# Optimization experiments

Hardware: AMD Instinct MI355X
Metric: run time of the kernel (lower is better)

Reference implementation:

```python
import jax, jax.numpy as jnp
import numpy as np
import math

D_MODEL = 512
N_HEADS = 8
D_FF = 2048
EPS = 1e-5

def _layernorm(x, g, b):
    m = jnp.mean(x, axis=-1, keepdims=True)
    v = jnp.var(x, axis=-1, keepdims=True)
    return (x - m) * jax.lax.rsqrt(v + EPS) * g + b

def setup_inputs() -> dict:
    key = jax.random.key(0)
    ks = jax.random.split(key, 8)
    d, dff = D_MODEL, D_FF
    s = lambda fan: 1.0 / math.sqrt(fan)
    return {
        "x": jax.random.normal(ks[0], (4, 2048, d), dtype=jnp.float32),
        "w_qkv": jax.random.normal(ks[1], (d, 3 * d), dtype=jnp.float32) * s(d),
        "b_qkv": jnp.zeros((3 * d,), dtype=jnp.float32),
        "w1": jax.random.normal(ks[2], (d, dff), dtype=jnp.float32) * s(d),
        "b1": jnp.zeros((dff,), dtype=jnp.float32),
        "w2": jax.random.normal(ks[3], (dff, d), dtype=jnp.float32) * s(dff),
        "b2": jnp.zeros((d,), dtype=jnp.float32),
        "g1": jnp.ones((d,), dtype=jnp.float32),
        "be1": jnp.zeros((d,), dtype=jnp.float32),
        "g2": jnp.ones((d,), dtype=jnp.float32),
        "be2": jnp.zeros((d,), dtype=jnp.float32),
    }

def reference(x, w_qkv, b_qkv, w1, b1, w2, b2, g1, be1, g2, be2):
    B, L, d = x.shape
    H = N_HEADS
    hd = d // H
    # Faithful to original: scale = 1/sqrt(hd), scores = qk / scale = qk * sqrt(hd)
    inv_scale = math.sqrt(hd)
    qkv = x @ w_qkv + b_qkv            # [B, L, 3d]
    q, k, v = jnp.split(qkv, 3, axis=-1)
    split_heads = lambda t: t.reshape(B, L, H, hd).transpose(0, 2, 1, 3)  # [B,H,L,hd]
    q, k, v = map(split_heads, (q, k, v))
    scores = jnp.einsum('bhqd,bhkd->bhqk', q, k) * inv_scale
    attn = jax.nn.softmax(scores, axis=-1)
    out = jnp.einsum('bhqk,bhkd->bhqd', attn, v)
    out = out.transpose(0, 2, 1, 3).reshape(B, L, d)
    x = _layernorm(x + out, g1, be1)
    ff = jax.nn.relu(x @ w1 + b1) @ w2 + b2
    return _layernorm(x + ff, g2, be2)
```

## Files before the change

kernel.cpp:

```cpp
#include <hip/hip_runtime.h>

typedef _Float16 f16;
typedef _Float16 f16x4 __attribute__((ext_vector_type(4)));
typedef _Float16 f16x8 __attribute__((ext_vector_type(8)));
typedef float    f32x4 __attribute__((ext_vector_type(4)));
typedef float    f32x16 __attribute__((ext_vector_type(16)));
typedef unsigned int u32x4 __attribute__((ext_vector_type(4)));

#define QK_SCALE 11.5416528f

__device__ __forceinline__ void g2l16(const void* g, void* l) {
  __builtin_amdgcn_global_load_lds(
      (__attribute__((address_space(1))) const unsigned int*)g,
      (__attribute__((address_space(3))) unsigned int*)l, 16, 0, 0);
}

__device__ __forceinline__ f32x4 mfma16(f16x8 a, f16x8 b, f32x4 c) {
  return __builtin_amdgcn_mfma_f32_16x16x32_f16(a, b, c, 0, 0, 0);
}
__device__ __forceinline__ f32x16 mfma32(f16x8 a, f16x8 b, f32x16 c) {
  return __builtin_amdgcn_mfma_f32_32x32x16_f16(a, b, c, 0, 0, 0);
}
__device__ __forceinline__ unsigned pkrtz(float a, float b) {
  auto t = __builtin_amdgcn_cvt_pkrtz(a, b);
  return *(unsigned*)&t;
}
__device__ __forceinline__ void swap32(unsigned& a, unsigned& b) {
  asm volatile("v_permlane32_swap_b32 %0, %1" : "+v"(a), "+v"(b));
}

__device__ __forceinline__ int swz64(int row, int c) { return row * 64 + ((c ^ (row & 7)) << 3); }
__device__ __forceinline__ int swz32(int row, int c) { return row * 32 + ((c ^ ((row >> 1) & 3)) << 3); }

__global__ __launch_bounds__(256) void k_split(const float* __restrict__ in,
                                               f16* __restrict__ hi, f16* __restrict__ lo, int n4) {
  int i = blockIdx.x * 256 + threadIdx.x;
  if (i >= n4) return;
  f32x4 v = ((const f32x4*)in)[i];
  f16x4 h, l;
#pragma unroll
  for (int j = 0; j < 4; ++j) {
    f16 hv = (f16)v[j];
    h[j] = hv;
    l[j] = (f16)(v[j] - (float)hv);
  }
  ((f16x4*)hi)[i] = h;
  ((f16x4*)lo)[i] = l;
}

template <bool WLO>
__global__ __launch_bounds__(256) void k_transpose_split(const float* __restrict__ in, int K, int N,
                                                         f16* __restrict__ oh, f16* __restrict__ ol) {
  __shared__ float t[32][33];
  const int tx = threadIdx.x, ty = threadIdx.y;
  const int n0 = blockIdx.x * 32, k0 = blockIdx.y * 32;
#pragma unroll
  for (int j = 0; j < 4; ++j)
    t[ty + j * 8][tx] = in[(size_t)(k0 + ty + j * 8) * N + n0 + tx];
  __syncthreads();
#pragma unroll
  for (int j = 0; j < 4; ++j) {
    float v = t[tx][ty + j * 8];
    f16 hv = (f16)v;
    size_t o = (size_t)(n0 + ty + j * 8) * K + k0 + tx;
    oh[o] = hv;
    if (WLO) ol[o] = (f16)(v - (float)hv);
  }
}

template <int EPI, bool SPLIT>
__global__ __launch_bounds__(256, SPLIT ? 2 : 3) void k_gemm(
    const f16* __restrict__ Ah, const f16* __restrict__ Al,
    const f16* __restrict__ Bh, const f16* __restrict__ Bl,
    const float* __restrict__ bias,
    float* __restrict__ outF, f16* __restrict__ outH,
    f16* __restrict__ oqh, f16* __restrict__ oql,
    f16* __restrict__ okh, f16* __restrict__ ovT,
    int M, int N, int K) {
  constexpr int NB = SPLIT ? 2 : 1;
  __shared__ f16 As[NB][128 * 32];
  __shared__ f16 Bs[NB][128 * 32];

  const int tid = threadIdx.x;
  const int bm = blockIdx.x, bn = blockIdx.y;
  const int w = tid >> 6, lane = tid & 63;
  const int wr = w >> 1, wc = w & 1;
  const int lrow = lane & 15, lgrp = lane >> 4;

  const bool useLo = SPLIT && !(EPI == 0 && bn >= 8);

  f32x4 acc[4][4] = {};

  const int nkt = K >> 5;
  for (int kt = 0; kt < nkt; ++kt) {
    __syncthreads();
    const int kk = kt << 5;
#pragma unroll
    for (int c = 0; c < 2; ++c) {
      const int i = tid + (c << 8);
      const int row = i >> 2;
      const int gch = ((i & 3) ^ ((i >> 3) & 3)) << 3;
      const size_t aoff = (size_t)(bm * 128 + row) * K + kk + gch;
      const size_t boff = (size_t)(bn * 128 + row) * K + kk + gch;
      g2l16(Ah + aoff, &As[0][i * 8]);
      g2l16(Bh + boff, &Bs[0][i * 8]);
      if (SPLIT)
        if (useLo) {
          g2l16(Al + aoff, &As[1][i * 8]);
          g2l16(Bl + boff, &Bs[1][i * 8]);
        }
    }
    __syncthreads();

    f16x8 a0[4], a1[4], b0[4], b1[4];
#pragma unroll
    for (int mf = 0; mf < 4; ++mf) {
      const int off = swz32(wr * 64 + mf * 16 + lrow, lgrp);
      a0[mf] = *(const f16x8*)&As[0][off];
      if (SPLIT)
        if (useLo) a1[mf] = *(const f16x8*)&As[SPLIT ? 1 : 0][off];
    }
#pragma unroll
    for (int nf = 0; nf < 4; ++nf) {
      const int off = swz32(wc * 64 + nf * 16 + lrow, lgrp);
      b0[nf] = *(const f16x8*)&Bs[0][off];
      if (SPLIT)
        if (useLo) b1[nf] = *(const f16x8*)&Bs[SPLIT ? 1 : 0][off];
    }
#pragma unroll
    for (int mf = 0; mf < 4; ++mf)
#pragma unroll
      for (int nf = 0; nf < 4; ++nf) {
        acc[mf][nf] = mfma16(a0[mf], b0[nf], acc[mf][nf]);
        if (SPLIT)
          if (useLo) {
            acc[mf][nf] = mfma16(a0[mf], b1[nf], acc[mf][nf]);
            acc[mf][nf] = mfma16(a1[mf], b0[nf], acc[mf][nf]);
          }
      }
  }

  const int rowbase = bm * 128 + wr * 64 + lgrp * 4;
  const int colbase = bn * 128 + wc * 64 + lrow;
#pragma unroll
  for (int mf = 0; mf < 4; ++mf) {
#pragma unroll
    for (int nf = 0; nf < 4; ++nf) {
      const int gc = colbase + nf * 16;
      const float bv = bias[gc];
#pragma unroll
      for (int r = 0; r < 4; ++r) {
        const int gr = rowbase + mf * 16 + r;
        const float val = acc[mf][nf][r] + bv;
        if (EPI == 0) {
          const int bb = gr >> 11, tok = gr & 2047;
          const int kind = gc >> 9, hh = (gc >> 6) & 7, dd = gc & 63;
          const size_t bhp = (size_t)((bb << 3) + hh);
          const size_t qidx = (bhp * 2048 + tok) * 64 + dd;
          if (kind == 0) {
            const float sv = val * QK_SCALE;
            const f16 hv = (f16)sv;
            oqh[qidx] = hv; oql[qidx] = (f16)(sv - (float)hv);
          } else if (kind == 1) {
            okh[qidx] = (f16)val;
          } else {
            ovT[(bhp * 64 + dd) * 2048 + tok] = (f16)val;
          }
        } else if (EPI == 1) {
          outH[(size_t)gr * N + gc] = (f16)fmaxf(val, 0.f);
        } else {
          outF[(size_t)gr * N + gc] = val;
        }
      }
    }
  }
}

__global__ __launch_bounds__(256, 2) void k_attn(
    const f16* __restrict__ Qh, const f16* __restrict__ Ql,
    const f16* __restrict__ Kh, const f16* __restrict__ Vt,
    float* __restrict__ out) {
  __shared__ f16 sK[3][64 * 64], sV[3][64 * 64];

  const int tid = threadIdx.x;
  const int wg = (blockIdx.x & 7) * 64 + (blockIdx.x >> 3);
  const int bh = wg >> 4, qt = wg & 15;
  const int w = tid >> 6, lane = tid & 63;
  const int lh = lane & 31, hh = lane >> 5;

  auto stage = [&](int b, int kt) {
    const size_t koff = ((size_t)bh * 2048 + (size_t)kt * 64) * 64;
    const size_t voff = (size_t)bh * 64 * 2048 + (size_t)kt * 64;
#pragma unroll
    for (int c = 0; c < 2; ++c) {
      const int i = tid + (c << 8);
      const int row = i >> 3;
      const int gch = ((i & 7) ^ (row & 7)) << 3;
      g2l16(Kh + koff + (size_t)row * 64 + gch, &sK[b][i * 8]);
      g2l16(Vt + voff + (size_t)row * 2048 + gch, &sV[b][i * 8]);
    }
  };

  stage(0, 0);
  stage(1, 1);

  const int qrow = qt * 128 + w * 32 + lh;
  const size_t qoff = ((size_t)bh * 2048 + qrow) * 64;
  f16x8 qh8[4], ql8[4];
#pragma unroll
  for (int d = 0; d < 4; ++d) {
    const size_t o = qoff + d * 16 + hh * 8;
    qh8[d] = *(const f16x8*)(Qh + o);
    ql8[d] = *(const f16x8*)(Ql + o);
  }

  float m_run = -3e38f;
  float l_run = 0.f;
  f32x16 oacc[2] = {};

  asm volatile("s_waitcnt vmcnt(4)" ::: "memory");
  __builtin_amdgcn_sched_barrier(0);
  __builtin_amdgcn_s_barrier();

  for (int kt = 0; kt < 32; ++kt) {
    const int cur = kt - (kt / 3) * 3;
    if (kt < 30) {
      const int nxt = (kt + 2) - ((kt + 2) / 3) * 3;
      stage(nxt, kt + 2);
    }

    f32x16 s[2] = {};
    __builtin_amdgcn_s_setprio(1);
#pragma unroll
    for (int d = 0; d < 4; ++d) {
      const f16x8 k0 = *(const f16x8*)&sK[cur][swz64(lh, d * 2 + hh)];
      const f16x8 k1 = *(const f16x8*)&sK[cur][swz64(32 + lh, d * 2 + hh)];
      s[0] = mfma32(k0, qh8[d], s[0]);
      s[0] = mfma32(k0, ql8[d], s[0]);
      s[1] = mfma32(k1, qh8[d], s[1]);
      s[1] = mfma32(k1, ql8[d], s[1]);
    }
    __builtin_amdgcn_s_setprio(0);

    float mt = s[0][0];
#pragma unroll
    for (int r = 0; r < 16; ++r) { mt = fmaxf(mt, s[0][r]); mt = fmaxf(mt, s[1][r]); }
    mt = fmaxf(mt, __shfl_xor(mt, 32, 64));
    float mcur = m_run;
    if (!__all(mt <= mcur + 8.0f)) {
      const float mnew = fmaxf(mcur, mt);
      const float corr = __builtin_amdgcn_exp2f(mcur - mnew);
      m_run = mnew;
      l_run *= corr;
      oacc[0] = oacc[0] * corr;
      oacc[1] = oacc[1] * corr;
      mcur = mnew;
    }
    float ps = 0.f;
    unsigned pk0[8], pk1[8];
#pragma unroll
    for (int i = 0; i < 8; ++i) {
      const float a0 = __builtin_amdgcn_exp2f(s[0][2 * i] - mcur);
      const float a1 = __builtin_amdgcn_exp2f(s[0][2 * i + 1] - mcur);
      const float b0 = __builtin_amdgcn_exp2f(s[1][2 * i] - mcur);
      const float b1 = __builtin_amdgcn_exp2f(s[1][2 * i + 1] - mcur);
      ps += (a0 + a1) + (b0 + b1);
      pk0[i] = pkrtz(a0, a1);
      pk1[i] = pkrtz(b0, b1);
    }
    ps += __shfl_xor(ps, 32, 64);
    l_run += ps;

    swap32(pk0[0], pk0[2]); swap32(pk0[1], pk0[3]);
    swap32(pk0[4], pk0[6]); swap32(pk0[5], pk0[7]);
    swap32(pk1[0], pk1[2]); swap32(pk1[1], pk1[3]);
    swap32(pk1[4], pk1[6]); swap32(pk1[5], pk1[7]);

    u32x4 pbu[4];
    pbu[0] = (u32x4){pk0[0], pk0[1], pk0[2], pk0[3]};
    pbu[1] = (u32x4){pk0[4], pk0[5], pk0[6], pk0[7]};
    pbu[2] = (u32x4){pk1[0], pk1[1], pk1[2], pk1[3]};
    pbu[3] = (u32x4){pk1[4], pk1[5], pk1[6], pk1[7]};

    __builtin_amdgcn_s_setprio(1);
#pragma unroll
    for (int s2 = 0; s2 < 4; ++s2) {
      const f16x8 pb = *(const f16x8*)&pbu[s2];
#pragma unroll
      for (int db = 0; db < 2; ++db) {
        const f16x8 v = *(const f16x8*)&sV[cur][swz64(db * 32 + lh, s2 * 2 + hh)];
        oacc[db] = mfma32(v, pb, oacc[db]);
      }
    }
    __builtin_amdgcn_s_setprio(0);

    if (kt < 30) {
      asm volatile("s_waitcnt vmcnt(4)" ::: "memory");
    } else {
      asm volatile("s_waitcnt vmcnt(0)" ::: "memory");
    }
    __builtin_amdgcn_sched_barrier(0);
    __builtin_amdgcn_s_barrier();
  }

  const int b = bh >> 3, hd = bh & 7;
  const float inv = 1.0f / l_run;
  const int trow = b * 2048 + qt * 128 + w * 32 + lh;
  float* po = out + (size_t)trow * 512 + hd * 64;
#pragma unroll
  for (int db = 0; db < 2; ++db)
#pragma unroll
    for (int rq = 0; rq < 4; ++rq) {
      f32x4 o;
#pragma unroll
      for (int j = 0; j < 4; ++j) o[j] = oacc[db][rq * 4 + j] * inv;
      *(f32x4*)(po + db * 32 + rq * 8 + hh * 4) = o;
    }
}

__global__ __launch_bounds__(64) void k_ln(const float* __restrict__ X, const float* __restrict__ R,
                                           const float* __restrict__ g, const float* __restrict__ be,
                                           float* __restrict__ outF, f16* __restrict__ outH) {
  const int row = blockIdx.x, t = threadIdx.x;
  const size_t base = (size_t)row * 512 + t * 8;
  f32x4 x0 = *(const f32x4*)(X + base);
  f32x4 x1 = *(const f32x4*)(X + base + 4);
  f32x4 r0 = *(const f32x4*)(R + base);
  f32x4 r1 = *(const f32x4*)(R + base + 4);
  x0 = x0 + r0;
  x1 = x1 + r1;
  float s = 0.f, ss = 0.f;
#pragma unroll
  for (int j = 0; j < 4; ++j) { s += x0[j] + x1[j]; ss += x0[j] * x0[j] + x1[j] * x1[j]; }
#pragma unroll
  for (int o = 32; o; o >>= 1) {
    s += __shfl_xor(s, o, 64);
    ss += __shfl_xor(ss, o, 64);
  }
  const float mean = s * (1.f / 512.f);
  const float var = ss * (1.f / 512.f) - mean * mean;
  const float rs = rsqrtf(var + 1e-5f);
  f32x4 g0 = *(const f32x4*)(g + t * 8);
  f32x4 g1v = *(const f32x4*)(g + t * 8 + 4);
  f32x4 b0 = *(const f32x4*)(be + t * 8);
  f32x4 b1 = *(const f32x4*)(be + t * 8 + 4);
  f32x4 y0 = (x0 - mean) * rs * g0 + b0;
  f32x4 y1 = (x1 - mean) * rs * g1v + b1;
  *(f32x4*)(outF + base) = y0;
  *(f32x4*)(outF + base + 4) = y1;
  if (outH != nullptr) {
    f16x8 hx;
#pragma unroll
    for (int j = 0; j < 4; ++j) { hx[j] = (f16)y0[j]; hx[j + 4] = (f16)y1[j]; }
    *(f16x8*)(outH + base) = hx;
  }
}

extern "C" void kernel_launch(void* const* d_in, const int* in_sizes, int n_in,
                              void* d_out, int out_size, void* d_ws, size_t ws_size,
                              hipStream_t stream) {
  (void)in_sizes; (void)n_in; (void)out_size;
  const float* x = (const float*)d_in[0];
  const float* w_qkv = (const float*)d_in[1];
  const float* b_qkv = (const float*)d_in[2];
  const float* w1 = (const float*)d_in[3];
  const float* b1 = (const float*)d_in[4];
  const float* w2 = (const float*)d_in[5];
  const float* b2 = (const float*)d_in[6];
  const float* g1 = (const float*)d_in[7];
  const float* be1 = (const float*)d_in[8];
  const float* g2 = (const float*)d_in[9];
  const float* be2 = (const float*)d_in[10];
  float* out = (float*)d_out;

  char* p = (char*)d_ws;
  auto take = [&](size_t bytes) {
    char* r = p;
    p += (bytes + 255) & ~(size_t)255;
    return r;
  };
  f16* xh = (f16*)take(8192ull * 512 * 2);
  f16* xl = (f16*)take(8192ull * 512 * 2);
  f16* wqkvTh = (f16*)take(1536ull * 512 * 2);
  f16* wqkvTl = (f16*)take(1536ull * 512 * 2);
  f16* w1T = (f16*)take(2048ull * 512 * 2);
  f16* w2T = (f16*)take(512ull * 2048 * 2);
  f16* qh = (f16*)take(32ull * 2048 * 64 * 2);
  f16* ql = (f16*)take(32ull * 2048 * 64 * 2);
  f16* kh = (f16*)take(32ull * 2048 * 64 * 2);
  f16* vT = (f16*)take(32ull * 64 * 2048 * 2);
  float* attn = (float*)take(8192ull * 512 * 4);
  float* x1f = (float*)take(8192ull * 512 * 4);
  f16* x1h = (f16*)take(8192ull * 512 * 2);
  f16* hbuf = qh;
  float* ffb = attn;

  if ((size_t)(p - (char*)d_ws) > ws_size) return;

  dim3 tb(32, 8);
  k_split<<<4096, 256, 0, stream>>>(x, xh, xl, 8192 * 512 / 4);
  k_transpose_split<true><<<dim3(1536 / 32, 512 / 32), tb, 0, stream>>>(w_qkv, 512, 1536, wqkvTh, wqkvTl);
  k_transpose_split<false><<<dim3(2048 / 32, 512 / 32), tb, 0, stream>>>(w1, 512, 2048, w1T, nullptr);
  k_transpose_split<false><<<dim3(512 / 32, 2048 / 32), tb, 0, stream>>>(w2, 2048, 512, w2T, nullptr);

  k_gemm<0, true><<<dim3(64, 12), 256, 0, stream>>>(xh, xl, wqkvTh, wqkvTl, b_qkv,
                                                    nullptr, nullptr, qh, ql, kh, vT,
                                                    8192, 1536, 512);
  k_attn<<<512, 256, 0, stream>>>(qh, ql, kh, vT, attn);
  k_ln<<<8192, 64, 0, stream>>>(x, attn, g1, be1, x1f, x1h);
  k_gemm<1, false><<<dim3(64, 16), 256, 0, stream>>>(x1h, nullptr, w1T, nullptr, b1,
                                                     nullptr, hbuf, nullptr, nullptr, nullptr, nullptr,
                                                     8192, 2048, 512);
  k_gemm<2, false><<<dim3(64, 4), 256, 0, stream>>>(hbuf, nullptr, w2T, nullptr, b2,
                                                    ffb, nullptr, nullptr, nullptr, nullptr, nullptr,
                                                    8192, 512, 2048);
  k_ln<<<8192, 64, 0, stream>>>(x1f, ffb, g2, be2, out, nullptr);
}
```

Before: 201.9 us.

## Software-pipeline QK^T ahead of softmax/PV with 4-deep K/V staging in attention

The attention loop is restructured so the QK^T MFMAs for the next key tile are issued before the softmax and PV of the current tile. This uses two score accumulators and a 4-buffer LDS ring prefetching three tiles ahead, and the Q register loads are moved ahead of the initial staging. The aim is to overlap matrix-core work with the exp/max VALU work and hide more global-load latency. In exchange it costs more LDS and registers, which may lower occupancy. Separately, the QKV GEMM now skips the low-part split for output columns from bn>=4 instead of bn>=8, which drops some correction MFMAs but may reduce precision for those columns.

Measured after the change: 194.1 us. -3.9%, faster.

```diff
diff --git a/kernel.cpp b/kernel.cpp
--- a/kernel.cpp
+++ b/kernel.cpp
@@ -87,7 +87,7 @@
   const int wr = w >> 1, wc = w & 1;
   const int lrow = lane & 15, lgrp = lane >> 4;
 
-  const bool useLo = SPLIT && !(EPI == 0 && bn >= 8);
+  const bool useLo = SPLIT && !(EPI == 0 && bn >= 4);
 
   f32x4 acc[4][4] = {};
 
@@ -180,13 +180,23 @@
     const f16* __restrict__ Qh, const f16* __restrict__ Ql,
     const f16* __restrict__ Kh, const f16* __restrict__ Vt,
     float* __restrict__ out) {
-  __shared__ f16 sK[3][64 * 64], sV[3][64 * 64];
+  __shared__ f16 sK[4][64 * 64], sV[4][64 * 64];
 
   const int tid = threadIdx.x;
   const int wg = (blockIdx.x & 7) * 64 + (blockIdx.x >> 3);
   const int bh = wg >> 4, qt = wg & 15;
   const int w = tid >> 6, lane = tid & 63;
   const int lh = lane & 31, hh = lane >> 5;
+
+  const int qrow = qt * 128 + w * 32 + lh;
+  const size_t qoff = ((size_t)bh * 2048 + qrow) * 64;
+  f16x8 qh8[4], ql8[4];
+#pragma unroll
+  for (int d = 0; d < 4; ++d) {
+    const size_t o = qoff + d * 16 + hh * 8;
+    qh8[d] = *(const f16x8*)(Qh + o);
+    ql8[d] = *(const f16x8*)(Ql + o);
+  }
 
   auto stage = [&](int b, int kt) {
     const size_t koff = ((size_t)bh * 2048 + (size_t)kt * 64) * 64;
@@ -203,45 +213,28 @@
 
   stage(0, 0);
   stage(1, 1);
-
-  const int qrow = qt * 128 + w * 32 + lh;
-  const size_t qoff = ((size_t)bh * 2048 + qrow) * 64;
-  f16x8 qh8[4], ql8[4];
-#pragma unroll
-  for (int d = 0; d < 4; ++d) {
-    const size_t o = qoff + d * 16 + hh * 8;
-    qh8[d] = *(const f16x8*)(Qh + o);
-    ql8[d] = *(const f16x8*)(Ql + o);
-  }
+  stage(2, 2);
 
   float m_run = -3e38f;
   float l_run = 0.f;
   f32x16 oacc[2] = {};
-
-  asm volatile("s_waitcnt vmcnt(4)" ::: "memory");
-  __builtin_amdgcn_sched_barrier(0);
-  __builtin_amdgcn_s_barrier();
-
-  for (int kt = 0; kt < 32; ++kt) {
-    const int cur = kt - (kt / 3) * 3;
-    if (kt < 30) {
-      const int nxt = (kt + 2) - ((kt + 2) / 3) * 3;
-      stage(nxt, kt + 2);
-    }
-
-    f32x16 s[2] = {};
+  f32x16 sA[2] = {}, sB[2] = {};
+
+  auto qk = [&](f32x16 (&s)[2], int bi) {
     __builtin_amdgcn_s_setprio(1);
 #pragma unroll
     for (int d = 0; d < 4; ++d) {
-      const f16x8 k0 = *(const f16x8*)&sK[cur][swz64(lh, d * 2 + hh)];
-      const f16x8 k1 = *(const f16x8*)&sK[cur][swz64(32 + lh, d * 2 + hh)];
+      const f16x8 k0 = *(const f16x8*)&sK[bi][swz64(lh, d * 2 + hh)];
+      const f16x8 k1 = *(const f16x8*)&sK[bi][swz64(32 + lh, d * 2 + hh)];
       s[0] = mfma32(k0, qh8[d], s[0]);
       s[0] = mfma32(k0, ql8[d], s[0]);
       s[1] = mfma32(k1, qh8[d], s[1]);
       s[1] = mfma32(k1, ql8[d], s[1]);
     }
     __builtin_amdgcn_s_setprio(0);
-
+  };
+
+  auto sm_pv = [&](f32x16 (&s)[2], int bi) {
     float mt = s[0][0];
 #pragma unroll
     for (int r = 0; r < 16; ++r) { mt = fmaxf(mt, s[0][r]); mt = fmaxf(mt, s[1][r]); }
@@ -270,6 +263,8 @@
     }
     ps += __shfl_xor(ps, 32, 64);
     l_run += ps;
+    s[0] = (f32x16){};
+    s[1] = (f32x16){};
 
     swap32(pk0[0], pk0[2]); swap32(pk0[1], pk0[3]);
     swap32(pk0[4], pk0[6]); swap32(pk0[5], pk0[7]);
@@ -288,19 +283,43 @@
       const f16x8 pb = *(const f16x8*)&pbu[s2];
 #pragma unroll
       for (int db = 0; db < 2; ++db) {
-        const f16x8 v = *(const f16x8*)&sV[cur][swz64(db * 32 + lh, s2 * 2 + hh)];
+        const f16x8 v = *(const f16x8*)&sV[bi][swz64(db * 32 + lh, s2 * 2 + hh)];
         oacc[db] = mfma32(v, pb, oacc[db]);
       }
     }
     __builtin_amdgcn_s_setprio(0);
-
-    if (kt < 30) {
+  };
+
+  auto endwait = [&](int t) {
+    if (t < 29) {
       asm volatile("s_waitcnt vmcnt(4)" ::: "memory");
     } else {
       asm volatile("s_waitcnt vmcnt(0)" ::: "memory");
     }
     __builtin_amdgcn_sched_barrier(0);
     __builtin_amdgcn_s_barrier();
+    __builtin_amdgcn_sched_barrier(0);
+  };
+
+  asm volatile("s_waitcnt vmcnt(4)" ::: "memory");
+  __builtin_amdgcn_sched_barrier(0);
+  __builtin_amdgcn_s_barrier();
+  __builtin_amdgcn_sched_barrier(0);
+  qk(sA, 0);
+
+  for (int t = 0; t < 32; t += 2) {
+    {
+      if (t + 1 < 32) qk(sB, (t + 1) & 3);
+      if (t + 3 < 32) stage((t + 3) & 3, t + 3);
+      sm_pv(sA, t & 3);
+      if (t + 1 < 32) endwait(t);
+    }
+    if (t + 1 < 32) {
+      if (t + 2 < 32) qk(sA, (t + 2) & 3);
+      if (t + 4 < 32) stage((t + 4) & 3, t + 4);
+      sm_pv(sB, (t + 1) & 3);
+      if (t + 2 < 32) endwait(t + 1);
+    }
   }
 
   const int b = bh >> 3, hd = bh & 7;
```
